# Kernel optimization log

Hardware: AMD Instinct MI355X
Metric: run time of the kernel (lower is better)

## Reference

```python
import jax, jax.numpy as jnp
import numpy as np

N_NODES = 100000
NEG_SLOPE = 0.2


def gat_conv(x, edge_index, W, a_src, a_dst, bias):
    """PyG GATConv, heads=1, concat, add_self_loops=True."""
    N = x.shape[0]
    loop = jnp.arange(N, dtype=edge_index.dtype)
    src = jnp.concatenate([edge_index[0], loop])  # message sources j
    dst = jnp.concatenate([edge_index[1], loop])  # message targets i
    h = x @ W                                      # [N, out]
    asrc = h @ a_src                               # [N]
    adst = h @ a_dst                               # [N]
    e = jax.nn.leaky_relu(asrc[src] + adst[dst], NEG_SLOPE)   # [E+N]
    m = jax.ops.segment_max(e, dst, num_segments=N)           # per-dst max
    w = jnp.exp(e - jax.lax.stop_gradient(m)[dst])
    denom = jax.ops.segment_sum(w, dst, num_segments=N)
    alpha = w / denom[dst]                                     # softmax per dst
    out = jax.ops.segment_sum(alpha[:, None] * h[src], dst, num_segments=N)
    return out + bias


def setup_inputs() -> dict:
    key = jax.random.key(0)
    ks = jax.random.split(key, 16)
    N, E, D = N_NODES, 3200000, 128
    x = jax.random.normal(ks[0], (N, D), dtype=jnp.float32)
    edge_index = jax.random.randint(ks[1], (2, E), 0, N, dtype=jnp.int64)
    def glorot(k, shape):
        fan = sum(shape)
        return jax.random.uniform(k, shape, jnp.float32, -1.0, 1.0) * np.sqrt(6.0 / fan)
    return {
        "x": x,
        "edge_index": edge_index,
        "W1": glorot(ks[2], (D, 16)),
        "a1_src": glorot(ks[3], (16,)),
        "a1_dst": glorot(ks[4], (16,)),
        "b1": jnp.zeros((16,), jnp.float32),
        "W2": glorot(ks[5], (16, 10)),
        "a2_src": glorot(ks[6], (10,)),
        "a2_dst": glorot(ks[7], (10,)),
        "b2": jnp.zeros((10,), jnp.float32),
        "Wl1": glorot(ks[8], (10, 10)),
        "bl1": jnp.zeros((10,), jnp.float32),
        "Wl2": glorot(ks[9], (10, 1)),
        "bl2": jnp.zeros((1,), jnp.float32),
    }


def reference(x, edge_index, W1, a1_src, a1_dst, b1, W2, a2_src, a2_dst, b2,
              Wl1, bl1, Wl2, bl2):
    h = gat_conv(x, edge_index, W1, a1_src, a1_dst, b1)
    h = jax.nn.relu(h)
    h = gat_conv(h, edge_index, W2, a2_src, a2_dst, b2)
    h = h @ Wl1 + bl1
    h = jax.nn.relu(h)
    return h @ Wl2 + bl2  # [N, 1]
```

## Files before the change

### kernel.cpp

```cpp
#include <hip/hip_runtime.h>
#include <hip/hip_fp16.h>


#define NEG 0.2f
#define FSH 7
#define BNODES 128
#define NSBMAX 1024
#define CAPB 4608
#define TILE 8192
#define PES 9

__device__ __forceinline__ float lrelu(float x) { return x > 0.0f ? x : NEG * x; }

__device__ __forceinline__ unsigned fenc(float f) {
    unsigned u = __float_as_uint(f);
    return (u & 0x80000000u) ? ~u : (u | 0x80000000u);
}
__device__ __forceinline__ float fdec(unsigned e) {
    return (e & 0x80000000u) ? __uint_as_float(e & 0x7FFFFFFFu) : __uint_as_float(~e);
}

__device__ __forceinline__ float4 ldh4(const __half* h, size_t off) {
    uint2 u = *(const uint2*)(h + off);
    __half2 a = *(__half2*)&u.x, b = *(__half2*)&u.y;
    float2 fa = __half22float2(a), fb = __half22float2(b);
    return make_float4(fa.x, fa.y, fb.x, fb.y);
}

__global__ __launch_bounds__(256) void k_init(unsigned* g, int* bcur, int NSB) {
    int i = blockIdx.x * 256 + threadIdx.x;
    if (i < NSB) bcur[i * 16] = i * CAPB;
    if (i < 2) g[i] = 0u;
}

__global__ __launch_bounds__(256) void k_gemm1(
    const float* __restrict__ x, const float* __restrict__ W1,
    const float* __restrict__ a1s, const float* __restrict__ a1d,
    __half* __restrict__ h1, float* __restrict__ s1, float* __restrict__ d1,
    unsigned* __restrict__ gmax, int N)
{
    __shared__ float sW[128 * 16];
    __shared__ float sx[64 * 132];
    __shared__ float wm[4];
    int tid = threadIdx.x;
    for (int i = tid; i < 2048; i += 256) sW[i] = W1[i];
    int node0 = blockIdx.x * 64;
    for (int i = tid; i < 64 * 32; i += 256) {
        int row = i >> 5, c4 = i & 31;
        int n = node0 + row;
        float4 v = make_float4(0.f, 0.f, 0.f, 0.f);
        if (n < N) v = ((const float4*)x)[(size_t)n * 32 + c4];
        *(float4*)&sx[row * 132 + c4 * 4] = v;
    }
    __syncthreads();

    int node = node0 + (tid >> 2);
    int grp  = tid & 3;
    const float* xr = &sx[(tid >> 2) * 132];
    float4 acc = make_float4(0.f, 0.f, 0.f, 0.f);
#pragma unroll 8
    for (int j = 0; j < 128; ++j) {
        float xv = xr[j];
        float4 w = *(const float4*)&sW[j * 16 + grp * 4];
        acc.x += xv * w.x; acc.y += xv * w.y; acc.z += xv * w.z; acc.w += xv * w.w;
    }
    float4 as = ((const float4*)a1s)[grp];
    float4 ad = ((const float4*)a1d)[grp];
    float sv = acc.x * as.x + acc.y * as.y + acc.z * as.z + acc.w * as.w;
    float dv = acc.x * ad.x + acc.y * ad.y + acc.z * ad.z + acc.w * ad.w;
    sv += __shfl_xor(sv, 1); sv += __shfl_xor(sv, 2);
    dv += __shfl_xor(dv, 1); dv += __shfl_xor(dv, 2);
    if (node < N) {
        __half2 p0 = __floats2half2_rn(acc.x, acc.y);
        __half2 p1 = __floats2half2_rn(acc.z, acc.w);
        uint2 u; u.x = *(unsigned*)&p0; u.y = *(unsigned*)&p1;
        *(uint2*)&h1[(size_t)node * 16 + grp * 4] = u;
        if (grp == 0) { s1[node] = sv; d1[node] = dv; }
    }
    float m = (node < N) ? sv : -3.4e38f;
#pragma unroll
    for (int off = 32; off >= 1; off >>= 1) m = fmaxf(m, __shfl_xor(m, off));
    if ((tid & 63) == 0) wm[tid >> 6] = m;
    __syncthreads();
    if (tid == 0) {
        float b = fmaxf(fmaxf(wm[0], wm[1]), fmaxf(wm[2], wm[3]));
        atomicMax(gmax, fenc(b));
    }
}

__global__ __launch_bounds__(512) void k_csplit(
    const int* __restrict__ esrc, const int* __restrict__ edst,
    int* __restrict__ bcur, unsigned* __restrict__ pairs, int E, int NSB)
{
    __shared__ unsigned lsrt[TILE];
    __shared__ int lhist[NSBMAX];
    __shared__ int lofs[NSBMAX];
    __shared__ int gbase[NSBMAX];
    __shared__ int wsum[8];
    int tid = threadIdx.x;
    int base = blockIdx.x * TILE;
    int tcnt = min(TILE, E - base);
    for (int i = tid; i < NSB; i += 512) lhist[i] = 0;
    __syncthreads();
    for (int i = tid; i < tcnt; i += 512)
        atomicAdd(&lhist[edst[base + i] >> FSH], 1);
    __syncthreads();
    int i0 = 2 * tid, i1 = i0 + 1;
    int a = (i0 < NSB) ? lhist[i0] : 0;
    int b = (i1 < NSB) ? lhist[i1] : 0;
    int s = a + b, pfx = s;
#pragma unroll
    for (int off = 1; off < 64; off <<= 1) {
        int t = __shfl_up(pfx, off, 64);
        if ((tid & 63) >= off) pfx += t;
    }
    if ((tid & 63) == 63) wsum[tid >> 6] = pfx;
    __syncthreads();
    int carry = 0;
    for (int w = 0; w < (tid >> 6); ++w) carry += wsum[w];
    int excl = pfx + carry - s;
    if (i0 < NSB) {
        lofs[i0] = excl;
        gbase[i0] = a ? atomicAdd(&bcur[i0 * 16], a) : 0;
    }
    if (i1 < NSB) {
        lofs[i1] = excl + a;
        gbase[i1] = b ? atomicAdd(&bcur[i1 * 16], b) : 0;
    }
    __syncthreads();
    if (i0 < NSB) lhist[i0] = lofs[i0];
    if (i1 < NSB) lhist[i1] = lofs[i1];
    __syncthreads();
    for (int i = tid; i < tcnt; i += 512) {
        int e = base + i;
        int d = edst[e], srcv = esrc[e];
        int pos = atomicAdd(&lhist[d >> FSH], 1);
        lsrt[pos] = ((unsigned)(d & (BNODES - 1)) << 17) | (unsigned)srcv;
    }
    __syncthreads();
    for (int i = tid; i < tcnt; i += 512) {
        int lo = 0, hi = NSB - 1;
        while (lo < hi) { int mid = (lo + hi + 1) >> 1; if (lofs[mid] <= i) lo = mid; else hi = mid - 1; }
        int gp = gbase[lo] + (i - lofs[lo]);
        if (gp < (lo + 1) * CAPB) pairs[gp] = lsrt[i];
    }
}

__global__ __launch_bounds__(512) void k_agg1(
    const int* __restrict__ bcur, const unsigned* __restrict__ pairs,
    const int* __restrict__ esrc, const int* __restrict__ edst,
    const float* __restrict__ s1, const float* __restrict__ d1, const __half* __restrict__ h1,
    const float* __restrict__ b1, const float* __restrict__ W2,
    const float* __restrict__ a2s, const float* __restrict__ a2d,
    __half* __restrict__ h2, float* __restrict__ s2, float* __restrict__ d2,
    const unsigned* __restrict__ gmax1p, unsigned* __restrict__ gmax2, int N, int E)
{
    __shared__ unsigned srt[CAPB];
    __shared__ float accs[BNODES * 17];
    __shared__ int lcnt[BNODES];
    __shared__ int lofs[BNODES + 1];
    __shared__ float dds[BNODES], mbs[BNODES];
    __shared__ float sW[160], sb[16], sas[16], sad[16];
    __shared__ int wsum[8];
    __shared__ float wm[8];

    int tid = threadIdx.x;
    int fb = blockIdx.x;
    if (tid < 160) sW[tid] = W2[tid];
    if (tid < 16) {
        sb[tid]  = b1[tid];
        sas[tid] = (tid < 10) ? a2s[tid] : 0.f;
        sad[tid] = (tid < 10) ? a2d[tid] : 0.f;
    }
    int node0 = fb << FSH;
    float g0 = fdec(*gmax1p);
    if (tid < BNODES) {
        int n = node0 + tid;
        float dd = (n < N) ? d1[n] : 0.f;
        dds[tid] = dd; mbs[tid] = lrelu(g0 + dd);
        lcnt[tid] = 0;
    }
    __syncthreads();

    int rbase = fb * CAPB;
    int cnt = bcur[fb * 16] - rbase;
    int gg = tid >> 2, q = tid & 3;

    if (cnt <= CAPB) {
        unsigned pe[PES];
#pragma unroll
        for (int u = 0; u < PES; ++u) {
            int i = tid + u * 512;
            bool ok = (i < cnt);
            pe[u] = ok ? pairs[rbase + i] : 0u;
            if (ok) atomicAdd(&lcnt[(pe[u] >> 17) & (BNODES - 1)], 1);
        }
        __syncthreads();
        int c = (tid < BNODES) ? lcnt[tid] : 0;
        int pfx = c;
#pragma unroll
        for (int off = 1; off < 64; off <<= 1) {
            int t = __shfl_up(pfx, off, 64);
            if ((tid & 63) >= off) pfx += t;
        }
        if ((tid & 63) == 63) wsum[tid >> 6] = pfx;
        __syncthreads();
        int carry = 0;
        for (int w = 0; w < (tid >> 6); ++w) carry += wsum[w];
        pfx += carry;
        if (tid < BNODES) { lofs[tid + 1] = pfx; lcnt[tid] = pfx - c; }
        if (tid == 0) lofs[0] = 0;
        __syncthreads();
#pragma unroll
        for (int u = 0; u < PES; ++u) {
            int i = tid + u * 512;
            if (i < cnt) {
                unsigned p = pe[u];
                int pos = atomicAdd(&lcnt[(p >> 17) & (BNODES - 1)], 1);
                srt[pos] = p & 0x1FFFF;
            }
        }
        __syncthreads();

        int n = node0 + gg;
        float4 accv; float den;
        if (n < N) {
            float w = __expf(lrelu(s1[n] + dds[gg]) - mbs[gg]);
            float4 hv = ldh4(h1, (size_t)n * 16 + 4 * q);
            accv = make_float4(w * hv.x, w * hv.y, w * hv.z, w * hv.w);
            den = w;
        } else { accv = make_float4(0.f, 0.f, 0.f, 0.f); den = 0.f; }
        {
            float dd = dds[gg], mb = mbs[gg];
            int j = lofs[gg], j1 = lofs[gg + 1];
            for (; j + 8 <= j1; j += 8) {
                int e0 = srt[j],     e1 = srt[j + 1], e2 = srt[j + 2], e3 = srt[j + 3];
                int e4 = srt[j + 4], e5 = srt[j + 5], e6 = srt[j + 6], e7 = srt[j + 7];
                int eqa = srt[j + q], eqb = srt[j + 4 + q];
                float4 H0 = ldh4(h1, (size_t)e0 * 16 + 4 * q);
                float4 H1 = ldh4(h1, (size_t)e1 * 16 + 4 * q);
                float4 H2 = ldh4(h1, (size_t)e2 * 16 + 4 * q);
                float4 H3 = ldh4(h1, (size_t)e3 * 16 + 4 * q);
                float4 H4 = ldh4(h1, (size_t)e4 * 16 + 4 * q);
                float4 H5 = ldh4(h1, (size_t)e5 * 16 + 4 * q);
                float4 H6 = ldh4(h1, (size_t)e6 * 16 + 4 * q);
                float4 H7 = ldh4(h1, (size_t)e7 * 16 + 4 * q);
                float sA = s1[eqa], sB = s1[eqb];
                float wA = __expf(lrelu(sA + dd) - mb);
                float wB = __expf(lrelu(sB + dd) - mb);
                float w0 = __shfl(wA, 0, 4), w1 = __shfl(wA, 1, 4);
                float w2 = __shfl(wA, 2, 4), w3 = __shfl(wA, 3, 4);
                float w4 = __shfl(wB, 0, 4), w5 = __shfl(wB, 1, 4);
                float w6 = __shfl(wB, 2, 4), w7 = __shfl(wB, 3, 4);
                accv.x += w0 * H0.x + w1 * H1.x + w2 * H2.x + w3 * H3.x
                        + w4 * H4.x + w5 * H5.x + w6 * H6.x + w7 * H7.x;
                accv.y += w0 * H0.y + w1 * H1.y + w2 * H2.y + w3 * H3.y
                        + w4 * H4.y + w5 * H5.y + w6 * H6.y + w7 * H7.y;
                accv.z += w0 * H0.z + w1 * H1.z + w2 * H2.z + w3 * H3.z
                        + w4 * H4.z + w5 * H5.z + w6 * H6.z + w7 * H7.z;
                accv.w += w0 * H0.w + w1 * H1.w + w2 * H2.w + w3 * H3.w
                        + w4 * H4.w + w5 * H5.w + w6 * H6.w + w7 * H7.w;
                den += ((w0 + w1) + (w2 + w3)) + ((w4 + w5) + (w6 + w7));
            }
            if (j + 4 <= j1) {
                int e0 = srt[j], e1 = srt[j + 1], e2 = srt[j + 2], e3 = srt[j + 3];
                float4 H0 = ldh4(h1, (size_t)e0 * 16 + 4 * q);
                float4 H1 = ldh4(h1, (size_t)e1 * 16 + 4 * q);
                float4 H2 = ldh4(h1, (size_t)e2 * 16 + 4 * q);
                float4 H3 = ldh4(h1, (size_t)e3 * 16 + 4 * q);
                int eq = srt[j + q];
                float wq = __expf(lrelu(s1[eq] + dd) - mb);
                float w0 = __shfl(wq, 0, 4), w1 = __shfl(wq, 1, 4);
                float w2 = __shfl(wq, 2, 4), w3 = __shfl(wq, 3, 4);
                accv.x += w0 * H0.x + w1 * H1.x + w2 * H2.x + w3 * H3.x;
                accv.y += w0 * H0.y + w1 * H1.y + w2 * H2.y + w3 * H3.y;
                accv.z += w0 * H0.z + w1 * H1.z + w2 * H2.z + w3 * H3.z;
                accv.w += w0 * H0.w + w1 * H1.w + w2 * H2.w + w3 * H3.w;
                den += (w0 + w1) + (w2 + w3);
                j += 4;
            }
            for (; j < j1; ++j) {
                int e0 = srt[j];
                float w0 = __expf(lrelu(s1[e0] + dd) - mb);
                float4 H0 = ldh4(h1, (size_t)e0 * 16 + 4 * q);
                accv.x += w0 * H0.x; accv.y += w0 * H0.y;
                accv.z += w0 * H0.z; accv.w += w0 * H0.w;
                den += w0;
            }
        }
        accs[gg * 17 + 4 * q + 0] = accv.x;
        accs[gg * 17 + 4 * q + 1] = accv.y;
        accs[gg * 17 + 4 * q + 2] = accv.z;
        accs[gg * 17 + 4 * q + 3] = accv.w;
        if (q == 0) accs[gg * 17 + 16] = den;
        __syncthreads();
    } else {
        for (int i = tid; i < BNODES * 17; i += 512) accs[i] = 0.f;
        __syncthreads();
        if (tid < BNODES) {
            int n = node0 + tid;
            if (n < N) {
                float w = __expf(lrelu(s1[n] + dds[tid]) - mbs[tid]);
#pragma unroll
                for (int t = 0; t < 16; ++t)
                    accs[tid * 17 + t] = w * __half2float(h1[(size_t)n * 16 + t]);
                accs[tid * 17 + 16] = w;
            }
        }
        __syncthreads();
        for (int i = tid; i < E; i += 512) {
            int d = edst[i];
            if ((d >> FSH) != fb) continue;
            int nl = d & (BNODES - 1), src = esrc[i];
            float w = __expf(lrelu(s1[src] + dds[nl]) - mbs[nl]);
#pragma unroll
            for (int t = 0; t < 16; ++t)
                atomicAdd(&accs[nl * 17 + t], w * __half2float(h1[(size_t)src * 16 + t]));
            atomicAdd(&accs[nl * 17 + 16], w);
        }
        __syncthreads();
    }

    int g = tid >> 4, k = tid & 15;
    float sval = -3.4e38f;
#pragma unroll
    for (int qq = 0; qq < 4; ++qq) {
        int nl = g * 4 + qq, nn = node0 + nl;
        if (nn >= N) continue;
        float inv = 1.f / accs[nl * 17 + 16];
        float o = fmaxf(accs[nl * 17 + k] * inv + sb[k], 0.f);
        float hh = 0.f;
#pragma unroll
        for (int kk = 0; kk < 16; ++kk) {
            float ov = __shfl(o, kk, 16);
            if (k < 10) hh += ov * sW[kk * 10 + k];
        }
        if (k >= 10) hh = 0.f;
        float ts = hh * sas[k];
        float td = hh * sad[k];
#pragma unroll
        for (int off = 1; off < 16; off <<= 1) {
            ts += __shfl_xor(ts, off, 16);
            td += __shfl_xor(td, off, 16);
        }
        h2[(size_t)nn * 16 + k] = __float2half_rn(hh);
        if (k == 0) { s2[nn] = ts; d2[nn] = td; }
        sval = fmaxf(sval, ts);
    }
    float m = sval;
#pragma unroll
    for (int off = 32; off >= 1; off >>= 1) m = fmaxf(m, __shfl_xor(m, off));
    if ((tid & 63) == 0) wm[tid >> 6] = m;
    __syncthreads();
    if (tid == 0) {
        float bmx = wm[0];
#pragma unroll
        for (int i = 1; i < 8; ++i) bmx = fmaxf(bmx, wm[i]);
        atomicMax(gmax2, fenc(bmx));
    }
}

__global__ __launch_bounds__(512) void k_agg2(
    const int* __restrict__ bcur, const unsigned* __restrict__ pairs,
    const int* __restrict__ esrc, const int* __restrict__ edst,
    const float* __restrict__ s2, const float* __restrict__ d2, const __half* __restrict__ h2,
    const float* __restrict__ b2, const float* __restrict__ Wl1, const float* __restrict__ bl1,
    const float* __restrict__ Wl2, const float* __restrict__ bl2,
    const unsigned* __restrict__ gmax2p, float* __restrict__ out, int N, int E)
{
    __shared__ unsigned srt[CAPB];
    __shared__ float accs[BNODES * 17];
    __shared__ int lcnt[BNODES];
    __shared__ int lofs[BNODES + 1];
    __shared__ float dds[BNODES], mbs[BNODES];
    __shared__ float sW1[100], sb1[16], sW2[16], sb2g[16];
    __shared__ float sbl2;
    __shared__ int wsum[8];

    int tid = threadIdx.x;
    int fb = blockIdx.x;
    if (tid < 100) sW1[tid] = Wl1[tid];
    if (tid < 16) {
        sb1[tid]  = (tid < 10) ? bl1[tid] : 0.f;
        sW2[tid]  = (tid < 10) ? Wl2[tid] : 0.f;
        sb2g[tid] = (tid < 10) ? b2[tid]  : 0.f;
    }
    if (tid == 0) sbl2 = bl2[0];
    int node0 = fb << FSH;
    float g0 = fdec(*gmax2p);
    if (tid < BNODES) {
        int n = node0 + tid;
        float dd = (n < N) ? d2[n] : 0.f;
        dds[tid] = dd; mbs[tid] = lrelu(g0 + dd);
        lcnt[tid] = 0;
    }
    __syncthreads();

    int rbase = fb * CAPB;
    int cnt = bcur[fb * 16] - rbase;
    int gg = tid >> 2, q = tid & 3;

    if (cnt <= CAPB) {
        unsigned pe[PES];
#pragma unroll
        for (int u = 0; u < PES; ++u) {
            int i = tid + u * 512;
            bool ok = (i < cnt);
            pe[u] = ok ? pairs[rbase + i] : 0u;
            if (ok) atomicAdd(&lcnt[(pe[u] >> 17) & (BNODES - 1)], 1);
        }
        __syncthreads();
        int c = (tid < BNODES) ? lcnt[tid] : 0;
        int pfx = c;
#pragma unroll
        for (int off = 1; off < 64; off <<= 1) {
            int t = __shfl_up(pfx, off, 64);
            if ((tid & 63) >= off) pfx += t;
        }
        if ((tid & 63) == 63) wsum[tid >> 6] = pfx;
        __syncthreads();
        int carry = 0;
        for (int w = 0; w < (tid >> 6); ++w) carry += wsum[w];
        pfx += carry;
        if (tid < BNODES) { lofs[tid + 1] = pfx; lcnt[tid] = pfx - c; }
        if (tid == 0) lofs[0] = 0;
        __syncthreads();
#pragma unroll
        for (int u = 0; u < PES; ++u) {
            int i = tid + u * 512;
            if (i < cnt) {
                unsigned p = pe[u];
                int pos = atomicAdd(&lcnt[(p >> 17) & (BNODES - 1)], 1);
                srt[pos] = p & 0x1FFFF;
            }
        }
        __syncthreads();

        int n = node0 + gg;
        float4 accv; float den;
        if (n < N) {
            float w = __expf(lrelu(s2[n] + dds[gg]) - mbs[gg]);
            float4 hv = ldh4(h2, (size_t)n * 16 + 4 * q);
            accv = make_float4(w * hv.x, w * hv.y, w * hv.z, w * hv.w);
            den = w;
        } else { accv = make_float4(0.f, 0.f, 0.f, 0.f); den = 0.f; }
        {
            float dd = dds[gg], mb = mbs[gg];
            int j = lofs[gg], j1 = lofs[gg + 1];
            for (; j + 8 <= j1; j += 8) {
                int e0 = srt[j],     e1 = srt[j + 1], e2 = srt[j + 2], e3 = srt[j + 3];
                int e4 = srt[j + 4], e5 = srt[j + 5], e6 = srt[j + 6], e7 = srt[j + 7];
                int eqa = srt[j + q], eqb = srt[j + 4 + q];
                float4 H0 = ldh4(h2, (size_t)e0 * 16 + 4 * q);
                float4 H1 = ldh4(h2, (size_t)e1 * 16 + 4 * q);
                float4 H2 = ldh4(h2, (size_t)e2 * 16 + 4 * q);
                float4 H3 = ldh4(h2, (size_t)e3 * 16 + 4 * q);
                float4 H4 = ldh4(h2, (size_t)e4 * 16 + 4 * q);
                float4 H5 = ldh4(h2, (size_t)e5 * 16 + 4 * q);
                float4 H6 = ldh4(h2, (size_t)e6 * 16 + 4 * q);
                float4 H7 = ldh4(h2, (size_t)e7 * 16 + 4 * q);
                float sA = s2[eqa], sB = s2[eqb];
                float wA = __expf(lrelu(sA + dd) - mb);
                float wB = __expf(lrelu(sB + dd) - mb);
                float w0 = __shfl(wA, 0, 4), w1 = __shfl(wA, 1, 4);
                float w2 = __shfl(wA, 2, 4), w3 = __shfl(wA, 3, 4);
                float w4 = __shfl(wB, 0, 4), w5 = __shfl(wB, 1, 4);
                float w6 = __shfl(wB, 2, 4), w7 = __shfl(wB, 3, 4);
                accv.x += w0 * H0.x + w1 * H1.x + w2 * H2.x + w3 * H3.x
                        + w4 * H4.x + w5 * H5.x + w6 * H6.x + w7 * H7.x;
                accv.y += w0 * H0.y + w1 * H1.y + w2 * H2.y + w3 * H3.y
                        + w4 * H4.y + w5 * H5.y + w6 * H6.y + w7 * H7.y;
                accv.z += w0 * H0.z + w1 * H1.z + w2 * H2.z + w3 * H3.z
                        + w4 * H4.z + w5 * H5.z + w6 * H6.z + w7 * H7.z;
                accv.w += w0 * H0.w + w1 * H1.w + w2 * H2.w + w3 * H3.w
                        + w4 * H4.w + w5 * H5.w + w6 * H6.w + w7 * H7.w;
                den += ((w0 + w1) + (w2 + w3)) + ((w4 + w5) + (w6 + w7));
            }
            if (j + 4 <= j1) {
                int e0 = srt[j], e1 = srt[j + 1], e2 = srt[j + 2], e3 = srt[j + 3];
                float4 H0 = ldh4(h2, (size_t)e0 * 16 + 4 * q);
                float4 H1 = ldh4(h2, (size_t)e1 * 16 + 4 * q);
                float4 H2 = ldh4(h2, (size_t)e2 * 16 + 4 * q);
                float4 H3 = ldh4(h2, (size_t)e3 * 16 + 4 * q);
                int eq = srt[j + q];
                float wq = __expf(lrelu(s2[eq] + dd) - mb);
                float w0 = __shfl(wq, 0, 4), w1 = __shfl(wq, 1, 4);
                float w2 = __shfl(wq, 2, 4), w3 = __shfl(wq, 3, 4);
                accv.x += w0 * H0.x + w1 * H1.x + w2 * H2.x + w3 * H3.x;
                accv.y += w0 * H0.y + w1 * H1.y + w2 * H2.y + w3 * H3.y;
                accv.z += w0 * H0.z + w1 * H1.z + w2 * H2.z + w3 * H3.z;
                accv.w += w0 * H0.w + w1 * H1.w + w2 * H2.w + w3 * H3.w;
                den += (w0 + w1) + (w2 + w3);
                j += 4;
            }
            for (; j < j1; ++j) {
                int e0 = srt[j];
                float w0 = __expf(lrelu(s2[e0] + dd) - mb);
                float4 H0 = ldh4(h2, (size_t)e0 * 16 + 4 * q);
                accv.x += w0 * H0.x; accv.y += w0 * H0.y;
                accv.z += w0 * H0.z; accv.w += w0 * H0.w;
                den += w0;
            }
        }
        accs[gg * 17 + 4 * q + 0] = accv.x;
        accs[gg * 17 + 4 * q + 1] = accv.y;
        accs[gg * 17 + 4 * q + 2] = accv.z;
        accs[gg * 17 + 4 * q + 3] = accv.w;
        if (q == 0) accs[gg * 17 + 16] = den;
        __syncthreads();
    } else {
        for (int i = tid; i < BNODES * 17; i += 512) accs[i] = 0.f;
        __syncthreads();
        if (tid < BNODES) {
            int n = node0 + tid;
            if (n < N) {
                float w = __expf(lrelu(s2[n] + dds[tid]) - mbs[tid]);
#pragma unroll
                for (int t = 0; t < 16; ++t)
                    accs[tid * 17 + t] = w * __half2float(h2[(size_t)n * 16 + t]);
                accs[tid * 17 + 16] = w;
            }
        }
        __syncthreads();
        for (int i = tid; i < E; i += 512) {
            int d = edst[i];
            if ((d >> FSH) != fb) continue;
            int nl = d & (BNODES - 1), src = esrc[i];
            float w = __expf(lrelu(s2[src] + dds[nl]) - mbs[nl]);
#pragma unroll
            for (int t = 0; t < 16; ++t)
                atomicAdd(&accs[nl * 17 + t], w * __half2float(h2[(size_t)src * 16 + t]));
            atomicAdd(&accs[nl * 17 + 16], w);
        }
        __syncthreads();
    }

    int g = tid >> 4, k = tid & 15;
    bool fk = k < 10;
#pragma unroll
    for (int qq = 0; qq < 4; ++qq) {
        int nl = g * 4 + qq, nn = node0 + nl;
        if (nn >= N) continue;
        float inv = 1.f / accs[nl * 17 + 16];
        float o = fk ? accs[nl * 17 + k] * inv + sb2g[k] : 0.f;
        float v = sb1[k];
#pragma unroll
        for (int kk = 0; kk < 10; ++kk) {
            float ov = __shfl(o, kk, 16);
            if (fk) v += ov * sW1[kk * 10 + k];
        }
        float t = fmaxf(v, 0.f);
        float cc = t * sW2[k];
#pragma unroll
        for (int off = 1; off < 16; off <<= 1) cc += __shfl_xor(cc, off, 16);
        if (k == 0) out[nn] = cc + sbl2;
    }
}

extern "C" void kernel_launch(void* const* d_in, const int* in_sizes, int n_in,
                              void* d_out, int out_size, void* d_ws, size_t ws_size,
                              hipStream_t stream)
{
    const float* x   = (const float*)d_in[0];
    const int*   ei  = (const int*)  d_in[1];
    const float* W1  = (const float*)d_in[2];
    const float* a1s = (const float*)d_in[3];
    const float* a1d = (const float*)d_in[4];
    const float* b1  = (const float*)d_in[5];
    const float* W2  = (const float*)d_in[6];
    const float* a2s = (const float*)d_in[7];
    const float* a2d = (const float*)d_in[8];
    const float* b2  = (const float*)d_in[9];
    const float* Wl1 = (const float*)d_in[10];
    const float* bl1 = (const float*)d_in[11];
    const float* Wl2 = (const float*)d_in[12];
    const float* bl2 = (const float*)d_in[13];

    int N = in_sizes[0] / 128;
    int E = in_sizes[1] / 2;
    const int* ei_src = ei;
    const int* ei_dst = ei + E;
    int NSB = (N + BNODES - 1) >> FSH;

    size_t Np = ((size_t)N + 3) & ~(size_t)3;
    size_t need_bytes = (16 + Np * 20) * 4 + (size_t)NSB * 16 * 4 + (size_t)NSB * CAPB * 4;
    if (ws_size < need_bytes) return;

    float*    ws    = (float*)d_ws;
    unsigned* gmax1 = (unsigned*)d_ws;
    unsigned* gmax2 = gmax1 + 1;
    __half* h1 = (__half*)(ws + 16);
    float* s1 = ws + 16 + Np * 8;
    float* d1 = s1 + Np;
    __half* h2 = (__half*)(d1 + Np);
    float* s2 = (float*)(h2) + Np * 8;
    float* d2 = s2 + Np;
    int* bcur = (int*)(d2 + Np);
    unsigned* pairs = (unsigned*)(bcur + (size_t)NSB * 16);

    hipLaunchKernelGGL(k_init, dim3((NSB + 255) / 256), dim3(256), 0, stream, gmax1, bcur, NSB);
    hipLaunchKernelGGL(k_gemm1, dim3((N + 63) / 64), dim3(256), 0, stream,
                       x, W1, a1s, a1d, h1, s1, d1, gmax1, N);
    hipLaunchKernelGGL(k_csplit, dim3((E + TILE - 1) / TILE), dim3(512), 0, stream,
                       ei_src, ei_dst, bcur, pairs, E, NSB);
    hipLaunchKernelGGL(k_agg1, dim3(NSB), dim3(512), 0, stream,
                       bcur, pairs, ei_src, ei_dst, s1, d1, h1, b1, W2, a2s, a2d,
                       h2, s2, d2, gmax1, gmax2, N, E);
    hipLaunchKernelGGL(k_agg2, dim3(NSB), dim3(512), 0, stream,
                       bcur, pairs, ei_src, ei_dst, s2, d2, h2, b2, Wl1, bl1, Wl2, bl2,
                       gmax2, (float*)d_out, N, E);
}
```

Measured before the change: 279.6 us.

## Halve bucket size and reuse agg1's per-node sorted edge lists in agg2

Node buckets shrink from 128 to 64 nodes, so there are twice as many aggregation blocks, each with 256 threads and less shared memory. The coarse-split scan now handles four buckets per thread. k_agg1 writes its locally sorted source list back into the pairs buffer, along with per-node offsets, so k_agg2 reads the sorted lists from global memory instead of redoing the count, scan and scatter. This removes a second local sort at the cost of an extra global write and global rather than LDS reads of edge indices in agg2. With the smaller bucket capacity, skewed buckets may fall back to the slow path more often.

```diff
diff --git a/kernel.cpp b/kernel.cpp
--- a/kernel.cpp
+++ b/kernel.cpp
@@ -3,12 +3,12 @@
 
 
 #define NEG 0.2f
-#define FSH 7
-#define BNODES 128
-#define NSBMAX 1024
-#define CAPB 4608
+#define FSH 6
+#define BNODES 64
+#define NSBMAX 2048
+#define CAPB 2560
 #define TILE 8192
-#define PES 9
+#define PES 10
 
 __device__ __forceinline__ float lrelu(float x) { return x > 0.0f ? x : NEG * x; }
 
@@ -105,10 +105,12 @@
     for (int i = tid; i < tcnt; i += 512)
         atomicAdd(&lhist[edst[base + i] >> FSH], 1);
     __syncthreads();
-    int i0 = 2 * tid, i1 = i0 + 1;
-    int a = (i0 < NSB) ? lhist[i0] : 0;
-    int b = (i1 < NSB) ? lhist[i1] : 0;
-    int s = a + b, pfx = s;
+    int i0 = 4 * tid;
+    int c0 = (i0 + 0 < NSB) ? lhist[i0 + 0] : 0;
+    int c1 = (i0 + 1 < NSB) ? lhist[i0 + 1] : 0;
+    int c2 = (i0 + 2 < NSB) ? lhist[i0 + 2] : 0;
+    int c3 = (i0 + 3 < NSB) ? lhist[i0 + 3] : 0;
+    int s = c0 + c1 + c2 + c3, pfx = s;
 #pragma unroll
     for (int off = 1; off < 64; off <<= 1) {
         int t = __shfl_up(pfx, off, 64);
@@ -119,17 +121,17 @@
     int carry = 0;
     for (int w = 0; w < (tid >> 6); ++w) carry += wsum[w];
     int excl = pfx + carry - s;
-    if (i0 < NSB) {
-        lofs[i0] = excl;
-        gbase[i0] = a ? atomicAdd(&bcur[i0 * 16], a) : 0;
-    }
-    if (i1 < NSB) {
-        lofs[i1] = excl + a;
-        gbase[i1] = b ? atomicAdd(&bcur[i1 * 16], b) : 0;
-    }
-    __syncthreads();
-    if (i0 < NSB) lhist[i0] = lofs[i0];
-    if (i1 < NSB) lhist[i1] = lofs[i1];
+    int cc[4] = { c0, c1, c2, c3 };
+    for (int u = 0; u < 4; ++u) {
+        int i = i0 + u;
+        if (i < NSB) {
+            lofs[i] = excl;
+            gbase[i] = cc[u] ? atomicAdd(&bcur[i * 16], cc[u]) : 0;
+            excl += cc[u];
+        }
+    }
+    __syncthreads();
+    for (int i = tid; i < NSB; i += 512) lhist[i] = lofs[i];
     __syncthreads();
     for (int i = tid; i < tcnt; i += 512) {
         int e = base + i;
@@ -146,8 +148,9 @@
     }
 }
 
-__global__ __launch_bounds__(512) void k_agg1(
-    const int* __restrict__ bcur, const unsigned* __restrict__ pairs,
+__global__ __launch_bounds__(256) void k_agg1(
+    const int* __restrict__ bcur, unsigned* __restrict__ pairs,
+    int* __restrict__ nodeofs,
     const int* __restrict__ esrc, const int* __restrict__ edst,
     const float* __restrict__ s1, const float* __restrict__ d1, const __half* __restrict__ h1,
     const float* __restrict__ b1, const float* __restrict__ W2,
@@ -161,8 +164,7 @@
     __shared__ int lofs[BNODES + 1];
     __shared__ float dds[BNODES], mbs[BNODES];
     __shared__ float sW[160], sb[16], sas[16], sad[16];
-    __shared__ int wsum[8];
-    __shared__ float wm[8];
+    __shared__ float wm[4];
 
     int tid = threadIdx.x;
     int fb = blockIdx.x;
@@ -190,30 +192,27 @@
         unsigned pe[PES];
 #pragma unroll
         for (int u = 0; u < PES; ++u) {
-            int i = tid + u * 512;
+            int i = tid + u * 256;
             bool ok = (i < cnt);
             pe[u] = ok ? pairs[rbase + i] : 0u;
             if (ok) atomicAdd(&lcnt[(pe[u] >> 17) & (BNODES - 1)], 1);
         }
         __syncthreads();
-        int c = (tid < BNODES) ? lcnt[tid] : 0;
-        int pfx = c;
-#pragma unroll
-        for (int off = 1; off < 64; off <<= 1) {
-            int t = __shfl_up(pfx, off, 64);
-            if ((tid & 63) >= off) pfx += t;
-        }
-        if ((tid & 63) == 63) wsum[tid >> 6] = pfx;
-        __syncthreads();
-        int carry = 0;
-        for (int w = 0; w < (tid >> 6); ++w) carry += wsum[w];
-        pfx += carry;
-        if (tid < BNODES) { lofs[tid + 1] = pfx; lcnt[tid] = pfx - c; }
-        if (tid == 0) lofs[0] = 0;
+        if (tid < 64) {
+            int c = lcnt[tid], pfx = c;
+#pragma unroll
+            for (int off = 1; off < 64; off <<= 1) {
+                int t = __shfl_up(pfx, off, 64);
+                if (tid >= off) pfx += t;
+            }
+            lofs[tid + 1] = pfx;
+            if (tid == 0) lofs[0] = 0;
+            lcnt[tid] = pfx - c;
+        }
         __syncthreads();
 #pragma unroll
         for (int u = 0; u < PES; ++u) {
-            int i = tid + u * 512;
+            int i = tid + u * 256;
             if (i < cnt) {
                 unsigned p = pe[u];
                 int pos = atomicAdd(&lcnt[(p >> 17) & (BNODES - 1)], 1);
@@ -221,6 +220,8 @@
             }
         }
         __syncthreads();
+        for (int i = tid; i < cnt; i += 256) pairs[rbase + i] = srt[i];
+        if (tid <= BNODES) nodeofs[fb * (BNODES + 1) + tid] = lofs[tid];
 
         int n = node0 + gg;
         float4 accv; float den;
@@ -295,7 +296,7 @@
         if (q == 0) accs[gg * 17 + 16] = den;
         __syncthreads();
     } else {
-        for (int i = tid; i < BNODES * 17; i += 512) accs[i] = 0.f;
+        for (int i = tid; i < BNODES * 17; i += 256) accs[i] = 0.f;
         __syncthreads();
         if (tid < BNODES) {
             int n = node0 + tid;
@@ -308,7 +309,7 @@
             }
         }
         __syncthreads();
-        for (int i = tid; i < E; i += 512) {
+        for (int i = tid; i < E; i += 256) {
             int d = edst[i];
             if ((d >> FSH) != fb) continue;
             int nl = d & (BNODES - 1), src = esrc[i];
@@ -353,29 +354,24 @@
     if ((tid & 63) == 0) wm[tid >> 6] = m;
     __syncthreads();
     if (tid == 0) {
-        float bmx = wm[0];
-#pragma unroll
-        for (int i = 1; i < 8; ++i) bmx = fmaxf(bmx, wm[i]);
+        float bmx = fmaxf(fmaxf(wm[0], wm[1]), fmaxf(wm[2], wm[3]));
         atomicMax(gmax2, fenc(bmx));
     }
 }
 
-__global__ __launch_bounds__(512) void k_agg2(
+__global__ __launch_bounds__(256) void k_agg2(
     const int* __restrict__ bcur, const unsigned* __restrict__ pairs,
+    const int* __restrict__ nodeofs,
     const int* __restrict__ esrc, const int* __restrict__ edst,
     const float* __restrict__ s2, const float* __restrict__ d2, const __half* __restrict__ h2,
     const float* __restrict__ b2, const float* __restrict__ Wl1, const float* __restrict__ bl1,
     const float* __restrict__ Wl2, const float* __restrict__ bl2,
     const unsigned* __restrict__ gmax2p, float* __restrict__ out, int N, int E)
 {
-    __shared__ unsigned srt[CAPB];
     __shared__ float accs[BNODES * 17];
-    __shared__ int lcnt[BNODES];
-    __shared__ int lofs[BNODES + 1];
     __shared__ float dds[BNODES], mbs[BNODES];
     __shared__ float sW1[100], sb1[16], sW2[16], sb2g[16];
     __shared__ float sbl2;
-    __shared__ int wsum[8];
 
     int tid = threadIdx.x;
     int fb = blockIdx.x;
@@ -392,7 +388,6 @@
         int n = node0 + tid;
         float dd = (n < N) ? d2[n] : 0.f;
         dds[tid] = dd; mbs[tid] = lrelu(g0 + dd);
-        lcnt[tid] = 0;
     }
     __syncthreads();
 
@@ -401,41 +396,8 @@
     int gg = tid >> 2, q = tid & 3;
 
     if (cnt <= CAPB) {
-        unsigned pe[PES];
-#pragma unroll
-        for (int u = 0; u < PES; ++u) {
-            int i = tid + u * 512;
-            bool ok = (i < cnt);
-            pe[u] = ok ? pairs[rbase + i] : 0u;
-            if (ok) atomicAdd(&lcnt[(pe[u] >> 17) & (BNODES - 1)], 1);
-        }
-        __syncthreads();
-        int c = (tid < BNODES) ? lcnt[tid] : 0;
-        int pfx = c;
-#pragma unroll
-        for (int off = 1; off < 64; off <<= 1) {
-            int t = __shfl_up(pfx, off, 64);
-            if ((tid & 63) >= off) pfx += t;
-        }
-        if ((tid & 63) == 63) wsum[tid >> 6] = pfx;
-        __syncthreads();
-        int carry = 0;
-        for (int w = 0; w < (tid >> 6); ++w) carry += wsum[w];
-        pfx += carry;
-        if (tid < BNODES) { lofs[tid + 1] = pfx; lcnt[tid] = pfx - c; }
-        if (tid == 0) lofs[0] = 0;
-        __syncthreads();
-#pragma unroll
-        for (int u = 0; u < PES; ++u) {
-            int i = tid + u * 512;
-            if (i < cnt) {
-                unsigned p = pe[u];
-                int pos = atomicAdd(&lcnt[(p >> 17) & (BNODES - 1)], 1);
-                srt[pos] = p & 0x1FFFF;
-            }
-        }
-        __syncthreads();
-
+        const unsigned* gs = pairs + rbase;
+        const int* nof = nodeofs + fb * (BNODES + 1);
         int n = node0 + gg;
         float4 accv; float den;
         if (n < N) {
@@ -446,11 +408,11 @@
         } else { accv = make_float4(0.f, 0.f, 0.f, 0.f); den = 0.f; }
         {
             float dd = dds[gg], mb = mbs[gg];
-            int j = lofs[gg], j1 = lofs[gg + 1];
+            int j = nof[gg], j1 = nof[gg + 1];
             for (; j + 8 <= j1; j += 8) {
-                int e0 = srt[j],     e1 = srt[j + 1], e2 = srt[j + 2], e3 = srt[j + 3];
-                int e4 = srt[j + 4], e5 = srt[j + 5], e6 = srt[j + 6], e7 = srt[j + 7];
-                int eqa = srt[j + q], eqb = srt[j + 4 + q];
+                int e0 = gs[j],     e1 = gs[j + 1], e2 = gs[j + 2], e3 = gs[j + 3];
+                int e4 = gs[j + 4], e5 = gs[j + 5], e6 = gs[j + 6], e7 = gs[j + 7];
+                int eqa = gs[j + q], eqb = gs[j + 4 + q];
                 float4 H0 = ldh4(h2, (size_t)e0 * 16 + 4 * q);
                 float4 H1 = ldh4(h2, (size_t)e1 * 16 + 4 * q);
                 float4 H2 = ldh4(h2, (size_t)e2 * 16 + 4 * q);
@@ -477,12 +439,12 @@
                 den += ((w0 + w1) + (w2 + w3)) + ((w4 + w5) + (w6 + w7));
             }
             if (j + 4 <= j1) {
-                int e0 = srt[j], e1 = srt[j + 1], e2 = srt[j + 2], e3 = srt[j + 3];
+                int e0 = gs[j], e1 = gs[j + 1], e2 = gs[j + 2], e3 = gs[j + 3];
                 float4 H0 = ldh4(h2, (size_t)e0 * 16 + 4 * q);
                 float4 H1 = ldh4(h2, (size_t)e1 * 16 + 4 * q);
                 float4 H2 = ldh4(h2, (size_t)e2 * 16 + 4 * q);
                 float4 H3 = ldh4(h2, (size_t)e3 * 16 + 4 * q);
-                int eq = srt[j + q];
+                int eq = gs[j + q];
                 float wq = __expf(lrelu(s2[eq] + dd) - mb);
                 float w0 = __shfl(wq, 0, 4), w1 = __shfl(wq, 1, 4);
                 float w2 = __shfl(wq, 2, 4), w3 = __shfl(wq, 3, 4);
@@ -494,7 +456,7 @@
                 j += 4;
             }
             for (; j < j1; ++j) {
-                int e0 = srt[j];
+                int e0 = gs[j];
                 float w0 = __expf(lrelu(s2[e0] + dd) - mb);
                 float4 H0 = ldh4(h2, (size_t)e0 * 16 + 4 * q);
                 accv.x += w0 * H0.x; accv.y += w0 * H0.y;
@@ -509,7 +471,7 @@
         if (q == 0) accs[gg * 17 + 16] = den;
         __syncthreads();
     } else {
-        for (int i = tid; i < BNODES * 17; i += 512) accs[i] = 0.f;
+        for (int i = tid; i < BNODES * 17; i += 256) accs[i] = 0.f;
         __syncthreads();
         if (tid < BNODES) {
             int n = node0 + tid;
@@ -522,7 +484,7 @@
             }
         }
         __syncthreads();
-        for (int i = tid; i < E; i += 512) {
+        for (int i = tid; i < E; i += 256) {
             int d = edst[i];
             if ((d >> FSH) != fb) continue;
             int nl = d & (BNODES - 1), src = esrc[i];
@@ -583,7 +545,8 @@
     int NSB = (N + BNODES - 1) >> FSH;
 
     size_t Np = ((size_t)N + 3) & ~(size_t)3;
-    size_t need_bytes = (16 + Np * 20) * 4 + (size_t)NSB * 16 * 4 + (size_t)NSB * CAPB * 4;
+    size_t need_bytes = (16 + Np * 20) * 4 + (size_t)NSB * 16 * 4
+                      + (size_t)NSB * CAPB * 4 + (size_t)NSB * (BNODES + 1) * 4;
     if (ws_size < need_bytes) return;
 
     float*    ws    = (float*)d_ws;
@@ -597,16 +560,17 @@
     float* d2 = s2 + Np;
     int* bcur = (int*)(d2 + Np);
     unsigned* pairs = (unsigned*)(bcur + (size_t)NSB * 16);
+    int* nodeofs = (int*)(pairs + (size_t)NSB * CAPB);
 
     hipLaunchKernelGGL(k_init, dim3((NSB + 255) / 256), dim3(256), 0, stream, gmax1, bcur, NSB);
     hipLaunchKernelGGL(k_gemm1, dim3((N + 63) / 64), dim3(256), 0, stream,
                        x, W1, a1s, a1d, h1, s1, d1, gmax1, N);
     hipLaunchKernelGGL(k_csplit, dim3((E + TILE - 1) / TILE), dim3(512), 0, stream,
                        ei_src, ei_dst, bcur, pairs, E, NSB);
-    hipLaunchKernelGGL(k_agg1, dim3(NSB), dim3(512), 0, stream,
-                       bcur, pairs, ei_src, ei_dst, s1, d1, h1, b1, W2, a2s, a2d,
+    hipLaunchKernelGGL(k_agg1, dim3(NSB), dim3(256), 0, stream,
+                       bcur, pairs, nodeofs, ei_src, ei_dst, s1, d1, h1, b1, W2, a2s, a2d,
                        h2, s2, d2, gmax1, gmax2, N, E);
-    hipLaunchKernelGGL(k_agg2, dim3(NSB), dim3(512), 0, stream,
-                       bcur, pairs, ei_src, ei_dst, s2, d2, h2, b2, Wl1, bl1, Wl2, bl2,
+    hipLaunchKernelGGL(k_agg2, dim3(NSB), dim3(256), 0, stream,
+                       bcur, pairs, nodeofs, ei_src, ei_dst, s2, d2, h2, b2, Wl1, bl1, Wl2, bl2,
                        gmax2, (float*)d_out, N, E);
 }
```

New measurement: 302.7 us. +8.3%, slower.
